# Kernel tuning notes

Measured on AMD Instinct MI355X. Metric: run time of the kernel, lower is better.

## Reference

```python
import jax, jax.numpy as jnp
import numpy as np

N_ENT, N_REL, D, E, NS, B = 100000, 200, 64, 1000000, 4096, 32


def setup_inputs() -> dict:
    key = jax.random.key(0)
    ks = jax.random.split(key, 20)
    s = 1.0 / np.sqrt(D)
    # rotational relation embeddings: [cos|sin ; cos|-sin] -> [2*N_REL, D]
    phases = (2 * np.pi * np.random.RandomState(0).rand(N_REL, D // 2)).astype(np.float32)
    rel = np.concatenate([
        np.concatenate([np.cos(phases), np.sin(phases)], -1),
        np.concatenate([np.cos(phases), -np.sin(phases)], -1)], 0)
    inp = {
        'ent_emb': jax.random.normal(ks[0], (N_ENT, D), jnp.float32) * s,
        'rel_emb': jnp.asarray(rel),
        'gcn_W': jax.random.normal(ks[1], (2, D, D), jnp.float32) * s,
        'gcn_b': jnp.zeros((2, D), jnp.float32),
        'mm_W0': jax.random.normal(ks[2], (3 * D, D), jnp.float32) * s,
        'mm_b0': jnp.zeros((D,), jnp.float32),
        'mm_W1': jax.random.normal(ks[3], (D, D), jnp.float32) * s,
        'mm_b1': jnp.zeros((D,), jnp.float32),
        'mm_Wadv': jax.random.normal(ks[4], (D, 3), jnp.float32) * s,
        'mm_badv': jnp.zeros((3,), jnp.float32),
        'mm_Wval': jax.random.normal(ks[5], (D, 1), jnp.float32) * s,
        'mm_bval': jnp.zeros((1,), jnp.float32),
        'ex_W0': jax.random.normal(ks[6], (D, D), jnp.float32) * s,
        'ex_b0': jnp.zeros((D,), jnp.float32),
        'ex_W1': jax.random.normal(ks[7], (D, D), jnp.float32) * s,
        'ex_b1': jnp.zeros((D,), jnp.float32),
        'ex_Wadv': jax.random.normal(ks[8], (D, 5), jnp.float32) * s,
        'ex_badv': jnp.zeros((5,), jnp.float32),
        'ex_Wval': jax.random.normal(ks[9], (D, 1), jnp.float32) * s,
        'ex_bval': jnp.zeros((1,), jnp.float32),
        'edge_index': jax.random.randint(ks[10], (2, E), 0, N_ENT, jnp.int32),
        'edge_type': jax.random.randint(ks[11], (E,), 0, 2 * N_REL, jnp.int32),
        'short_idx': jax.random.randint(ks[12], (NS,), 0, E, jnp.int32),
        'agent_idx': jax.random.randint(ks[13], (B,), 0, N_ENT, jnp.int32),
    }
    return inp


def _dueling_mlp(h, W0, b0, W1, b1, Wadv, badv, Wval, bval):
    h = jax.nn.relu(h @ W0 + b0)
    h = jax.nn.relu(h @ W1 + b1)
    adv = h @ Wadv + badv
    val = h @ Wval + bval
    return val + adv - adv.mean(-1, keepdims=True)


def reference(ent_emb, rel_emb, gcn_W, gcn_b, mm_W0, mm_b0, mm_W1, mm_b1,
              mm_Wadv, mm_badv, mm_Wval, mm_bval, ex_W0, ex_b0, ex_W1, ex_b1,
              ex_Wadv, ex_badv, ex_Wval, ex_bval,
              edge_index, edge_type, short_idx, agent_idx):
    n = ent_emb.shape[0]
    src, dst = edge_index[0], edge_index[1]
    x = ent_emb
    for l in range(gcn_W.shape[0]):  # GCNConv, normalize=False, no self-loops
        msg = (x @ gcn_W[l])[src]                      # [E, D] gather-transform
        x = jax.ops.segment_sum(msg, dst, num_segments=n) + gcn_b[l]
        x = jax.nn.relu(x)                             # dropout is identity in eval
    # memory-management head: concat(head, relation, tail) for short-term triples
    h_mm = jnp.concatenate([x[src[short_idx]], rel_emb[edge_type[short_idx]],
                            x[dst[short_idx]]], axis=-1)  # [NS, 3D]
    q_mm = _dueling_mlp(h_mm, mm_W0, mm_b0, mm_W1, mm_b1, mm_Wadv, mm_badv, mm_Wval, mm_bval)
    # explore head: agent-node embedding
    q_ex = _dueling_mlp(x[agent_idx], ex_W0, ex_b0, ex_W1, ex_b1, ex_Wadv, ex_badv, ex_Wval, ex_bval)
    return q_mm, q_ex
```

## Files before the change

### kernel.cpp

```cpp
#include <hip/hip_runtime.h>

#define DD 64
#define CAP 32

typedef short bf16x8 __attribute__((ext_vector_type(8)));
typedef float f32x4 __attribute__((ext_vector_type(4)));

static __device__ __forceinline__ unsigned short f2bf(float f) {
  unsigned u = __float_as_uint(f);
  return (unsigned short)((u + 0x7fffu + ((u >> 16) & 1u)) >> 16);
}
static __device__ __forceinline__ unsigned pack2bf(float lo, float hi) {
  return (((unsigned)f2bf(hi)) << 16) | (unsigned)f2bf(lo);
}


__global__ __launch_bounds__(256) void k_zero(
    int* __restrict__ f4, int nf4, int* __restrict__ cnt, int N) {
  const int i = blockIdx.x * 256 + threadIdx.x;
  if (i < nf4) f4[i] = 0;
  if (i < N) cnt[i] = 0;
}

__global__ __launch_bounds__(256) void k_flag2(
    const int* __restrict__ sidx, const int* __restrict__ src,
    const int* __restrict__ dst, const int* __restrict__ aidx,
    unsigned char* __restrict__ flags, int NS, int B) {
  const int i = blockIdx.x * 256 + threadIdx.x;
  if (i < NS) {
    int e = sidx[i];
    flags[src[e]] = 1;
    flags[dst[e]] = 1;
  } else if (i < NS + B) {
    flags[aidx[i - NS]] = 1;
  }
}

__device__ __forceinline__ void gemm_body(
    const float* __restrict__ x, const float* __restrict__ W,
    unsigned short* __restrict__ yh, int N, int bid, int nB) {
  __shared__ unsigned short wt[DD * DD];
  __shared__ float ys[4][16][68];
  for (int i = threadIdx.x; i < DD * DD; i += 256) {
    int k = i >> 6, n = i & 63;
    wt[n * DD + k] = f2bf(W[i]);
  }
  __syncthreads();
  const int wave = threadIdx.x >> 6;
  const int lane = threadIdx.x & 63;
  const int g = lane >> 4;
  const int m = lane & 15;
  bf16x8 bfr[8];
#pragma unroll
  for (int nt = 0; nt < 4; ++nt)
#pragma unroll
    for (int m2 = 0; m2 < 2; ++m2) {
      const int base = (nt * 16 + m) * DD + 4 * g + 32 * m2;
      ushort4 lo = *(const ushort4*)&wt[base];
      ushort4 hi = *(const ushort4*)&wt[base + 16];
      bf16x8 f;
      f[0] = (short)lo.x; f[1] = (short)lo.y; f[2] = (short)lo.z; f[3] = (short)lo.w;
      f[4] = (short)hi.x; f[5] = (short)hi.y; f[6] = (short)hi.z; f[7] = (short)hi.w;
      bfr[nt * 2 + m2] = f;
    }
  const int tiles = (N + 15) / 16;
  for (int t = bid * 4 + wave; t < tiles; t += nB * 4) {
    const int row = t * 16 + m;
    const int rsafe = (row < N) ? row : (N - 1);
    const float* xr = x + (size_t)rsafe * DD + 4 * g;
    float4 a0 = *(const float4*)(xr + 0);
    float4 a1 = *(const float4*)(xr + 16);
    float4 a2 = *(const float4*)(xr + 32);
    float4 a3 = *(const float4*)(xr + 48);
    bf16x8 af0, af1;
    af0[0] = (short)f2bf(a0.x); af0[1] = (short)f2bf(a0.y);
    af0[2] = (short)f2bf(a0.z); af0[3] = (short)f2bf(a0.w);
    af0[4] = (short)f2bf(a1.x); af0[5] = (short)f2bf(a1.y);
    af0[6] = (short)f2bf(a1.z); af0[7] = (short)f2bf(a1.w);
    af1[0] = (short)f2bf(a2.x); af1[1] = (short)f2bf(a2.y);
    af1[2] = (short)f2bf(a2.z); af1[3] = (short)f2bf(a2.w);
    af1[4] = (short)f2bf(a3.x); af1[5] = (short)f2bf(a3.y);
    af1[6] = (short)f2bf(a3.z); af1[7] = (short)f2bf(a3.w);
    f32x4 acc0 = {0.f, 0.f, 0.f, 0.f}, acc1 = acc0, acc2 = acc0, acc3 = acc0;
    acc0 = __builtin_amdgcn_mfma_f32_16x16x32_bf16(af0, bfr[0], acc0, 0, 0, 0);
    acc0 = __builtin_amdgcn_mfma_f32_16x16x32_bf16(af1, bfr[1], acc0, 0, 0, 0);
    acc1 = __builtin_amdgcn_mfma_f32_16x16x32_bf16(af0, bfr[2], acc1, 0, 0, 0);
    acc1 = __builtin_amdgcn_mfma_f32_16x16x32_bf16(af1, bfr[3], acc1, 0, 0, 0);
    acc2 = __builtin_amdgcn_mfma_f32_16x16x32_bf16(af0, bfr[4], acc2, 0, 0, 0);
    acc2 = __builtin_amdgcn_mfma_f32_16x16x32_bf16(af1, bfr[5], acc2, 0, 0, 0);
    acc3 = __builtin_amdgcn_mfma_f32_16x16x32_bf16(af0, bfr[6], acc3, 0, 0, 0);
    acc3 = __builtin_amdgcn_mfma_f32_16x16x32_bf16(af1, bfr[7], acc3, 0, 0, 0);
#pragma unroll
    for (int r = 0; r < 4; ++r) {
      ys[wave][4 * g + r][0 * 16 + m] = acc0[r];
      ys[wave][4 * g + r][1 * 16 + m] = acc1[r];
      ys[wave][4 * g + r][2 * 16 + m] = acc2[r];
      ys[wave][4 * g + r][3 * 16 + m] = acc3[r];
    }
    if (row < N) {
      unsigned short* yr = yh + (size_t)row * DD + g * 16;
      const float* s = &ys[wave][m][g * 16];
      uint4 olo, ohi;
      olo.x = pack2bf(s[0], s[1]);
      olo.y = pack2bf(s[2], s[3]);
      olo.z = pack2bf(s[4], s[5]);
      olo.w = pack2bf(s[6], s[7]);
      ohi.x = pack2bf(s[8], s[9]);
      ohi.y = pack2bf(s[10], s[11]);
      ohi.z = pack2bf(s[12], s[13]);
      ohi.w = pack2bf(s[14], s[15]);
      *(uint4*)yr = olo;
      *(uint4*)(yr + 8) = ohi;
    }
  }
}

__global__ __launch_bounds__(256) void k_pre2(
    const float* __restrict__ x, const float* __restrict__ W,
    unsigned short* __restrict__ yh, int N, int GB,
    const int* __restrict__ src, const int* __restrict__ dst,
    unsigned char* __restrict__ flags, int E) {
  const int bid = blockIdx.x;
  if (bid < GB) {
    gemm_body(x, W, yh, N, bid, GB);
  } else {
    const int T = (gridDim.x - GB) * 256;
    int e = (bid - GB) * 256 + threadIdx.x;
#pragma unroll
    for (int j = 0; j < 4; ++j, e += T) {
      if (e < E && (flags[dst[e]] & 1)) {
        int s = src[e];
        flags[s] = flags[s] | 2;
      }
    }
  }
}

__global__ __launch_bounds__(256) void k_fillcnt(
    const int* __restrict__ src, const int* __restrict__ dst,
    const unsigned char* __restrict__ flags, int* __restrict__ cnt,
    int* __restrict__ csr, int E) {
  const int T = gridDim.x * 256;
  const int e0 = blockIdx.x * 256 + threadIdx.x;
  int dd[4], ss[4];
  bool act[4];
#pragma unroll
  for (int j = 0; j < 4; ++j) {
    const int e = e0 + j * T;
    act[j] = false;
    if (e < E) {
      dd[j] = dst[e];
      ss[j] = src[e];
      act[j] = flags[dd[j]] != 0;
    }
  }
#pragma unroll
  for (int j = 0; j < 4; ++j) {
    if (act[j]) {
      int slot = atomicAdd(&cnt[dd[j]], 1);
      if (slot < CAP) csr[dd[j] * CAP + slot] = ss[j];
    }
  }
}

__global__ __launch_bounds__(256) void k_gather_h(
    const unsigned short* __restrict__ yh, const int* __restrict__ cnt,
    const int* __restrict__ csr, const float* __restrict__ b,
    float* __restrict__ outp, int N, const unsigned char* __restrict__ flags,
    int bit) {
  const int wave = threadIdx.x >> 6;
  const int lane = threadIdx.x & 63;
  const int h = lane >> 5;
  const int c = lane & 31;
  const int n = blockIdx.x * 4 + wave;
  if (n >= N) return;
  if (!(flags[n] & bit)) return;
  const float b0r = b[2 * c];
  const float b1r = b[2 * c + 1];
  int i = n * CAP;
  int c2 = cnt[n];
  c2 = (c2 < CAP) ? c2 : CAP;
  const int end = i + c2;
  float a0 = 0.f, a1 = 0.f;
  for (; i + 8 <= end; i += 8) {
    int ib = __builtin_amdgcn_readfirstlane(i);
    int sA = csr[ib + 0 + h];
    int sB = csr[ib + 2 + h];
    int sC = csr[ib + 4 + h];
    int sD = csr[ib + 6 + h];
    unsigned vA = *(const unsigned*)&yh[(size_t)sA * DD + 2 * c];
    unsigned vB = *(const unsigned*)&yh[(size_t)sB * DD + 2 * c];
    unsigned vC = *(const unsigned*)&yh[(size_t)sC * DD + 2 * c];
    unsigned vD = *(const unsigned*)&yh[(size_t)sD * DD + 2 * c];
    a0 += (__uint_as_float(vA << 16) + __uint_as_float(vB << 16)) +
          (__uint_as_float(vC << 16) + __uint_as_float(vD << 16));
    a1 += (__uint_as_float(vA & 0xffff0000u) + __uint_as_float(vB & 0xffff0000u)) +
          (__uint_as_float(vC & 0xffff0000u) + __uint_as_float(vD & 0xffff0000u));
  }
  for (; i + 2 <= end; i += 2) {
    int sA = csr[__builtin_amdgcn_readfirstlane(i) + h];
    unsigned vA = *(const unsigned*)&yh[(size_t)sA * DD + 2 * c];
    a0 += __uint_as_float(vA << 16);
    a1 += __uint_as_float(vA & 0xffff0000u);
  }
  if (i < end && h == 0) {
    int sA = csr[i];
    unsigned vA = *(const unsigned*)&yh[(size_t)sA * DD + 2 * c];
    a0 += __uint_as_float(vA << 16);
    a1 += __uint_as_float(vA & 0xffff0000u);
  }
  a0 += __shfl_xor(a0, 32);
  a1 += __shfl_xor(a1, 32);
  if (h == 0) {
    float2 r;
    r.x = fmaxf(a0 + b0r, 0.f);
    r.y = fmaxf(a1 + b1r, 0.f);
    *(float2*)&outp[(size_t)n * DD + 2 * c] = r;
  }
}

__global__ __launch_bounds__(256) void k_gather_s(
    const float* __restrict__ x1, const int* __restrict__ cnt,
    const int* __restrict__ csr, unsigned short* __restrict__ s2, int N,
    const unsigned char* __restrict__ flags) {
  const int wave = threadIdx.x >> 6;
  const int lane = threadIdx.x & 63;
  const int n = blockIdx.x * 4 + wave;
  if (n >= N) return;
  if (!(flags[n] & 1)) return;
  int i = n * CAP;
  int c2 = cnt[n];
  c2 = (c2 < CAP) ? c2 : CAP;
  const int end = i + c2;
  float a = 0.f;
  for (; i + 4 <= end; i += 4) {
    int ib = __builtin_amdgcn_readfirstlane(i);
    int p0 = csr[ib + 0];
    int p1 = csr[ib + 1];
    int p2 = csr[ib + 2];
    int p3 = csr[ib + 3];
    a += (x1[(size_t)p0 * DD + lane] + x1[(size_t)p1 * DD + lane]) +
         (x1[(size_t)p2 * DD + lane] + x1[(size_t)p3 * DD + lane]);
  }
  for (; i < end; ++i) {
    int p = csr[__builtin_amdgcn_readfirstlane(i)];
    a += x1[(size_t)p * DD + lane];
  }
  s2[(size_t)n * DD + lane] = f2bf(a);
}

__global__ __launch_bounds__(256) void k_xform(
    const unsigned short* __restrict__ s2, const float* __restrict__ W1,
    const float* __restrict__ b1, const unsigned char* __restrict__ flags,
    float* __restrict__ outp, int N) {
  __shared__ __align__(16) float Ws[DD * DD];
  __shared__ __align__(16) float xs[4][DD];
  for (int i = threadIdx.x; i < DD * DD; i += 256) Ws[i] = W1[i];
  __syncthreads();
  const int wave = threadIdx.x >> 6;
  const int lane = threadIdx.x & 63;
  const float br = b1[lane];
  for (int n = blockIdx.x * 4 + wave; n < N; n += gridDim.x * 4) {
    if (!(flags[n] & 1)) continue;
    unsigned u = s2[(size_t)n * DD + lane];
    xs[wave][lane] = __uint_as_float(u << 16);
    float acc = br;
#pragma unroll
    for (int k4 = 0; k4 < 16; ++k4) {
      float4 h4 = *(const float4*)&xs[wave][k4 * 4];
      acc = fmaf(h4.x, Ws[(k4 * 4 + 0) * DD + lane], acc);
      acc = fmaf(h4.y, Ws[(k4 * 4 + 1) * DD + lane], acc);
      acc = fmaf(h4.z, Ws[(k4 * 4 + 2) * DD + lane], acc);
      acc = fmaf(h4.w, Ws[(k4 * 4 + 3) * DD + lane], acc);
    }
    outp[(size_t)n * DD + lane] = fmaxf(acc, 0.f);
  }
}

__global__ __launch_bounds__(256) void k_transform(
    const float* __restrict__ x, const float* __restrict__ W,
    float* __restrict__ y, int n_rows, int relu_in) {
  __shared__ __align__(16) float Ws[DD * DD];
  __shared__ __align__(16) float xs[4][DD];
  for (int i = threadIdx.x; i < DD * DD; i += 256) Ws[i] = W[i];
  __syncthreads();
  const int wave = threadIdx.x >> 6;
  const int lane = threadIdx.x & 63;
  for (int n = blockIdx.x * 4 + wave; n < n_rows; n += gridDim.x * 4) {
    float xv = x[n * DD + lane];
    if (relu_in) xv = fmaxf(xv, 0.f);
    xs[wave][lane] = xv;
    float acc = 0.f;
#pragma unroll
    for (int k4 = 0; k4 < DD / 4; ++k4) {
      float4 h4 = *(const float4*)&xs[wave][k4 * 4];
      acc = fmaf(h4.x, Ws[(k4 * 4 + 0) * DD + lane], acc);
      acc = fmaf(h4.y, Ws[(k4 * 4 + 1) * DD + lane], acc);
      acc = fmaf(h4.z, Ws[(k4 * 4 + 2) * DD + lane], acc);
      acc = fmaf(h4.w, Ws[(k4 * 4 + 3) * DD + lane], acc);
    }
    y[n * DD + lane] = acc;
  }
}

__global__ __launch_bounds__(256) void k_init_bias(
    float4* __restrict__ acc, const float* __restrict__ b, int total4) {
  const float4* b4 = (const float4*)b;
  for (int i = blockIdx.x * blockDim.x + threadIdx.x; i < total4;
       i += gridDim.x * blockDim.x)
    acc[i] = b4[i & 15];
}

__global__ __launch_bounds__(256) void k_scatter(
    const float* __restrict__ y, const int* __restrict__ src,
    const int* __restrict__ dst, float* __restrict__ acc, int E) {
  const int total = E * 16;
  for (int i = blockIdx.x * blockDim.x + threadIdx.x; i < total;
       i += gridDim.x * blockDim.x) {
    int e = i >> 4;
    int d4 = (i & 15) << 2;
    int s = src[e], dd = dst[e];
    float4 v = *(const float4*)&y[s * DD + d4];
    float* ap = &acc[dd * DD + d4];
    unsafeAtomicAdd(ap + 0, v.x);
    unsafeAtomicAdd(ap + 1, v.y);
    unsafeAtomicAdd(ap + 2, v.z);
    unsafeAtomicAdd(ap + 3, v.w);
  }
}

__global__ __launch_bounds__(256) void k_relu_inplace(float* __restrict__ p, int n) {
  for (int i = blockIdx.x * blockDim.x + threadIdx.x; i < n;
       i += gridDim.x * blockDim.x)
    p[i] = fmaxf(p[i], 0.f);
}

__global__ __launch_bounds__(256) void k_heads(
    const float* __restrict__ xact, const float* __restrict__ rel,
    const int* __restrict__ src, const int* __restrict__ dst,
    const int* __restrict__ etype, const int* __restrict__ sidx,
    const float* __restrict__ mmW0, const float* __restrict__ mmB0,
    const float* __restrict__ mmW1, const float* __restrict__ mmB1,
    const float* __restrict__ mmWa, const float* __restrict__ mmBa,
    const float* __restrict__ mmWv, const float* __restrict__ mmBv,
    const float* __restrict__ exW0, const float* __restrict__ exB0,
    const float* __restrict__ exW1, const float* __restrict__ exB1,
    const float* __restrict__ exWa, const float* __restrict__ exBa,
    const float* __restrict__ exWv, const float* __restrict__ exBv,
    const int* __restrict__ aidx, float* __restrict__ q_mm,
    float* __restrict__ q_ex, int NS, int B, int MB) {
  __shared__ __align__(16) float W0s[192 * DD];
  __shared__ float Wadvs[DD * 5], Wvals[DD], b0s[DD], b1s[DD], badvs[5];
  __shared__ __align__(16) float hs[4][192];
  __shared__ __align__(16) float h1s[4][DD];
  const int wave = threadIdx.x >> 6;
  const int lane = threadIdx.x & 63;
  if (blockIdx.x < MB) {
    for (int i = threadIdx.x; i < 192 * DD; i += 256) W0s[i] = mmW0[i];
    for (int i = threadIdx.x; i < DD * 3; i += 256) Wadvs[i] = mmWa[i];
    if (threadIdx.x < DD) {
      Wvals[threadIdx.x] = mmWv[threadIdx.x];
      b0s[threadIdx.x] = mmB0[threadIdx.x];
      b1s[threadIdx.x] = mmB1[threadIdx.x];
    }
    if (threadIdx.x < 3) badvs[threadIdx.x] = mmBa[threadIdx.x];
    __syncthreads();
    const float bv = mmBv[0];
    for (int i = blockIdx.x * 4 + wave; i < NS; i += MB * 4) {
      int e = sidx[i];
      int s = src[e], dd = dst[e], t = etype[e];
      hs[wave][lane] = fmaxf(xact[s * DD + lane], 0.f);
      hs[wave][64 + lane] = rel[t * DD + lane];
      hs[wave][128 + lane] = fmaxf(xact[dd * DD + lane], 0.f);
      float acc = b0s[lane];
#pragma unroll
      for (int k4 = 0; k4 < 48; ++k4) {
        float4 h4 = *(const float4*)&hs[wave][k4 * 4];
        acc = fmaf(h4.x, W0s[(k4 * 4 + 0) * DD + lane], acc);
        acc = fmaf(h4.y, W0s[(k4 * 4 + 1) * DD + lane], acc);
        acc = fmaf(h4.z, W0s[(k4 * 4 + 2) * DD + lane], acc);
        acc = fmaf(h4.w, W0s[(k4 * 4 + 3) * DD + lane], acc);
      }
      h1s[wave][lane] = fmaxf(acc, 0.f);
      float acc2 = b1s[lane];
#pragma unroll
      for (int k4 = 0; k4 < 16; ++k4) {
        float4 h4 = *(const float4*)&h1s[wave][k4 * 4];
        acc2 = fmaf(h4.x, mmW1[(k4 * 4 + 0) * DD + lane], acc2);
        acc2 = fmaf(h4.y, mmW1[(k4 * 4 + 1) * DD + lane], acc2);
        acc2 = fmaf(h4.z, mmW1[(k4 * 4 + 2) * DD + lane], acc2);
        acc2 = fmaf(h4.w, mmW1[(k4 * 4 + 3) * DD + lane], acc2);
      }
      float h2 = fmaxf(acc2, 0.f);
      float p0 = h2 * Wadvs[lane * 3 + 0];
      float p1 = h2 * Wadvs[lane * 3 + 1];
      float p2 = h2 * Wadvs[lane * 3 + 2];
      float pv = h2 * Wvals[lane];
#pragma unroll
      for (int off = 32; off; off >>= 1) {
        p0 += __shfl_xor(p0, off);
        p1 += __shfl_xor(p1, off);
        p2 += __shfl_xor(p2, off);
        pv += __shfl_xor(pv, off);
      }
      if (lane == 0) {
        float a0 = p0 + badvs[0], a1 = p1 + badvs[1], a2 = p2 + badvs[2];
        float val = pv + bv;
        float m = (a0 + a1 + a2) * (1.f / 3.f);
        q_mm[i * 3 + 0] = val + a0 - m;
        q_mm[i * 3 + 1] = val + a1 - m;
        q_mm[i * 3 + 2] = val + a2 - m;
      }
    }
  } else {
    float* W1s = W0s + DD * DD;
    for (int i = threadIdx.x; i < DD * DD; i += 256) {
      W0s[i] = exW0[i];
      W1s[i] = exW1[i];
    }
    for (int i = threadIdx.x; i < DD * 5; i += 256) Wadvs[i] = exWa[i];
    if (threadIdx.x < DD) {
      Wvals[threadIdx.x] = exWv[threadIdx.x];
      b0s[threadIdx.x] = exB0[threadIdx.x];
      b1s[threadIdx.x] = exB1[threadIdx.x];
    }
    if (threadIdx.x < 5) badvs[threadIdx.x] = exBa[threadIdx.x];
    __syncthreads();
    const float bv = exBv[0];
    const int i = (blockIdx.x - MB) * 4 + wave;
    if (i >= B) return;
    int n = aidx[i];
    hs[wave][lane] = fmaxf(xact[n * DD + lane], 0.f);
    float acc = b0s[lane];
#pragma unroll
    for (int k4 = 0; k4 < 16; ++k4) {
      float4 h4 = *(const float4*)&hs[wave][k4 * 4];
      acc = fmaf(h4.x, W0s[(k4 * 4 + 0) * DD + lane], acc);
      acc = fmaf(h4.y, W0s[(k4 * 4 + 1) * DD + lane], acc);
      acc = fmaf(h4.z, W0s[(k4 * 4 + 2) * DD + lane], acc);
      acc = fmaf(h4.w, W0s[(k4 * 4 + 3) * DD + lane], acc);
    }
    h1s[wave][lane] = fmaxf(acc, 0.f);
    float acc2 = b1s[lane];
#pragma unroll
    for (int k4 = 0; k4 < 16; ++k4) {
      float4 h4 = *(const float4*)&h1s[wave][k4 * 4];
      acc2 = fmaf(h4.x, W1s[(k4 * 4 + 0) * DD + lane], acc2);
      acc2 = fmaf(h4.y, W1s[(k4 * 4 + 1) * DD + lane], acc2);
      acc2 = fmaf(h4.z, W1s[(k4 * 4 + 2) * DD + lane], acc2);
      acc2 = fmaf(h4.w, W1s[(k4 * 4 + 3) * DD + lane], acc2);
    }
    float h2 = fmaxf(acc2, 0.f);
    float p[6];
#pragma unroll
    for (int c = 0; c < 5; ++c) p[c] = h2 * Wadvs[lane * 5 + c];
    p[5] = h2 * Wvals[lane];
#pragma unroll
    for (int off = 32; off; off >>= 1)
#pragma unroll
      for (int c = 0; c < 6; ++c) p[c] += __shfl_xor(p[c], off);
    if (lane == 0) {
      float a[5];
      float m = 0.f;
#pragma unroll
      for (int c = 0; c < 5; ++c) {
        a[c] = p[c] + badvs[c];
        m += a[c];
      }
      m *= 0.2f;
      float val = p[5] + bv;
#pragma unroll
      for (int c = 0; c < 5; ++c) q_ex[i * 5 + c] = val + a[c] - m;
    }
  }
}

extern "C" void kernel_launch(void* const* d_in, const int* in_sizes, int n_in,
                              void* d_out, int out_size, void* d_ws, size_t ws_size,
                              hipStream_t stream) {
  const float* ent = (const float*)d_in[0];
  const float* rel = (const float*)d_in[1];
  const float* gcnW = (const float*)d_in[2];
  const float* gcnB = (const float*)d_in[3];
  const float* mmW0 = (const float*)d_in[4];
  const float* mmB0 = (const float*)d_in[5];
  const float* mmW1 = (const float*)d_in[6];
  const float* mmB1 = (const float*)d_in[7];
  const float* mmWa = (const float*)d_in[8];
  const float* mmBa = (const float*)d_in[9];
  const float* mmWv = (const float*)d_in[10];
  const float* mmBv = (const float*)d_in[11];
  const float* exW0 = (const float*)d_in[12];
  const float* exB0 = (const float*)d_in[13];
  const float* exW1 = (const float*)d_in[14];
  const float* exB1 = (const float*)d_in[15];
  const float* exWa = (const float*)d_in[16];
  const float* exBa = (const float*)d_in[17];
  const float* exWv = (const float*)d_in[18];
  const float* exBv = (const float*)d_in[19];
  const int* eidx = (const int*)d_in[20];
  const int* etype = (const int*)d_in[21];
  const int* sidx = (const int*)d_in[22];
  const int* aidx = (const int*)d_in[23];

  const int N = in_sizes[0] / DD;
  const int E = in_sizes[20] / 2;
  const int NS = in_sizes[22];
  const int B = in_sizes[23];
  const int* src = eidx;
  const int* dst = eidx + E;

  float* bufA = (float*)d_ws;
  float* bufB = bufA + (size_t)N * DD;
  int* cnt = (int*)(bufB + (size_t)N * DD);
  unsigned char* flags = (unsigned char*)(cnt + N);
  unsigned short* yh = (unsigned short*)bufA;
  int* csr = (int*)d_ws + (size_t)N * DD / 2;
  const int nf4 = (N + 3) / 4;
  const size_t need = ((size_t)2 * N * DD + (size_t)N) * 4 + (size_t)nf4 * 4;

  float* q_mm = (float*)d_out;
  float* q_ex = q_mm + (size_t)NS * 3;

  dim3 blk(256);
  const int GB = 512;
  const int EB4 = (E + 1023) / 1024;
  const int FB4 = ((E + 3) / 4 + 255) / 256;
  const int MB = 256;
  const int XB = (B + 3) / 4;

  if (ws_size >= need) {
    k_zero<<<(N + 255) / 256, blk, 0, stream>>>((int*)flags, nf4, cnt, N);
    k_flag2<<<(NS + B + 255) / 256, blk, 0, stream>>>(sidx, src, dst, aidx, flags,
                                                      NS, B);
    k_pre2<<<GB + EB4, blk, 0, stream>>>(ent, gcnW, yh, N, GB, src, dst, flags, E);
    k_fillcnt<<<FB4, blk, 0, stream>>>(src, dst, flags, cnt, csr, E);
    k_gather_h<<<(N + 3) / 4, blk, 0, stream>>>(yh, cnt, csr, gcnB, bufB, N, flags,
                                                2);
    k_gather_s<<<(N + 3) / 4, blk, 0, stream>>>(bufB, cnt, csr, yh, N, flags);
    k_xform<<<512, blk, 0, stream>>>(yh, gcnW + DD * DD, gcnB + DD, flags, bufB, N);
    k_heads<<<MB + XB, blk, 0, stream>>>(bufB, rel, src, dst, etype, sidx, mmW0,
                                         mmB0, mmW1, mmB1, mmWa, mmBa, mmWv, mmBv,
                                         exW0, exB0, exW1, exB1, exWa, exBa, exWv,
                                         exBv, aidx, q_mm, q_ex, NS, B, MB);
  } else {
    float* tmp = bufA;
    k_transform<<<1024, blk, 0, stream>>>(ent, gcnW, tmp, N, 0);
    k_init_bias<<<1024, blk, 0, stream>>>((float4*)bufB, gcnB, N * 16);
    k_scatter<<<2048, blk, 0, stream>>>(tmp, src, dst, bufB, E);
    k_transform<<<1024, blk, 0, stream>>>(bufB, gcnW + DD * DD, tmp, N, 1);
    k_init_bias<<<1024, blk, 0, stream>>>((float4*)bufB, gcnB + DD, N * 16);
    k_scatter<<<2048, blk, 0, stream>>>(tmp, src, dst, bufB, E);
    k_relu_inplace<<<1024, blk, 0, stream>>>(bufB, N * DD);
    k_heads<<<MB + XB, blk, 0, stream>>>(bufB, rel, src, dst, etype, sidx, mmW0,
                                         mmB0, mmW1, mmB1, mmWa, mmBa, mmWv, mmBv,
                                         exW0, exB0, exW1, exB1, exWa, exBa, exWv,
                                         exBv, aidx, q_mm, q_ex, NS, B, MB);
  }
}
```

Before: 142.5 us.

## Partition CSR fill atomics by destination region per XCD

Replaces the edge-parallel CSR fill kernel with one where blocks are grouped by XCD (blockIdx mod 8). Each group scans all edges but only processes destinations whose region index (dst >> 12, mod 8) matches its XCD. The aim is to keep atomic counter updates and CSR writes local to one XCD's L2 and avoid cross-die atomic traffic. The cost is that every group rereads the full dst array, multiplying edge-index read traffic by the number of XCDs.

```diff
diff --git a/kernel.cpp b/kernel.cpp
--- a/kernel.cpp
+++ b/kernel.cpp
@@ -2,6 +2,8 @@
 
 #define DD 64
 #define CAP 32
+#define NXCD 8
+#define REG_SHIFT 12
 
 typedef short bf16x8 __attribute__((ext_vector_type(8)));
 typedef float f32x4 __attribute__((ext_vector_type(4)));
@@ -136,29 +138,18 @@
   }
 }
 
-__global__ __launch_bounds__(256) void k_fillcnt(
+__global__ __launch_bounds__(256) void k_fill_xcd(
     const int* __restrict__ src, const int* __restrict__ dst,
     const unsigned char* __restrict__ flags, int* __restrict__ cnt,
     int* __restrict__ csr, int E) {
-  const int T = gridDim.x * 256;
-  const int e0 = blockIdx.x * 256 + threadIdx.x;
-  int dd[4], ss[4];
-  bool act[4];
-#pragma unroll
-  for (int j = 0; j < 4; ++j) {
-    const int e = e0 + j * T;
-    act[j] = false;
-    if (e < E) {
-      dd[j] = dst[e];
-      ss[j] = src[e];
-      act[j] = flags[dd[j]] != 0;
-    }
-  }
-#pragma unroll
-  for (int j = 0; j < 4; ++j) {
-    if (act[j]) {
-      int slot = atomicAdd(&cnt[dd[j]], 1);
-      if (slot < CAP) csr[dd[j] * CAP + slot] = ss[j];
+  const int xcd = blockIdx.x & (NXCD - 1);
+  const int grank = blockIdx.x >> 3;
+  const int step = (gridDim.x >> 3) * 256;
+  for (int e = grank * 256 + threadIdx.x; e < E; e += step) {
+    int d = dst[e];
+    if (((d >> REG_SHIFT) & (NXCD - 1)) == xcd && flags[d]) {
+      int slot = atomicAdd(&cnt[d], 1);
+      if (slot < CAP) csr[d * CAP + slot] = src[e];
     }
   }
 }
@@ -525,7 +516,7 @@
   dim3 blk(256);
   const int GB = 512;
   const int EB4 = (E + 1023) / 1024;
-  const int FB4 = ((E + 3) / 4 + 255) / 256;
+  const int FB = 2048;
   const int MB = 256;
   const int XB = (B + 3) / 4;
 
@@ -534,7 +525,7 @@
     k_flag2<<<(NS + B + 255) / 256, blk, 0, stream>>>(sidx, src, dst, aidx, flags,
                                                       NS, B);
     k_pre2<<<GB + EB4, blk, 0, stream>>>(ent, gcnW, yh, N, GB, src, dst, flags, E);
-    k_fillcnt<<<FB4, blk, 0, stream>>>(src, dst, flags, cnt, csr, E);
+    k_fill_xcd<<<FB, blk, 0, stream>>>(src, dst, flags, cnt, csr, E);
     k_gather_h<<<(N + 3) / 4, blk, 0, stream>>>(yh, cnt, csr, gcnB, bufB, N, flags,
                                                 2);
     k_gather_s<<<(N + 3) / 4, blk, 0, stream>>>(bufB, cnt, csr, yh, N, flags);
```

New measurement: 140.9 us. About the same (-1.2%).
